# Optimization experiments

Hardware: AMD Instinct MI355X
Metric: run time of the kernel (lower is better)

## Reference

```python
import jax, jax.numpy as jnp
import numpy as np

NUM_USER = 100000
NUM_ENTITY = 1000000
NUM_RELATION = 60
DIM = 32
N_NEIGHBOR = 16
N_ITER = 2
BATCH = 8192


def setup_inputs() -> dict:
    key = jax.random.key(0)
    ks = jax.random.split(key, 9)
    users = jax.random.randint(ks[0], (BATCH,), 0, NUM_USER)
    items = jax.random.randint(ks[1], (BATCH,), 0, NUM_ENTITY)
    entity_emb = jax.random.normal(ks[2], (NUM_ENTITY, DIM), dtype=jnp.float32) * 0.1
    relation_emb = jax.random.normal(ks[3], (NUM_RELATION, DIM), dtype=jnp.float32) * 0.1
    adj_entity = jax.random.randint(ks[4], (NUM_ENTITY, N_NEIGHBOR), 0, NUM_ENTITY)
    adj_relation = jax.random.randint(ks[5], (NUM_ENTITY, N_NEIGHBOR), 0, NUM_RELATION)
    user_history = jax.random.randint(ks[6], (NUM_USER, N_NEIGHBOR), 0, NUM_ENTITY)
    W = jax.random.normal(ks[7], (DIM, DIM), dtype=jnp.float32) / np.sqrt(DIM)
    b = jnp.zeros((DIM,), dtype=jnp.float32)
    return {"users": users, "items": items, "entity_emb": entity_emb,
            "relation_emb": relation_emb, "adj_entity": adj_entity,
            "adj_relation": adj_relation, "user_history": user_history,
            "W": W, "b": b}


def reference(users, items, entity_emb, relation_emb, adj_entity, adj_relation, user_history, W, b):
    B = users.shape[0]
    d = entity_emb.shape[1]
    K = adj_entity.shape[1]

    # user embedding: mean-pool over gathered history item embeddings
    hist = user_history[users]                         # [B, K]
    user_emb = entity_emb[hist].mean(axis=1)           # [B, d]

    # multi-hop neighbor expansion (irregular gathers)
    entities = [items.reshape(B, 1)]
    relations = []
    for h in range(N_ITER):
        e = adj_entity[entities[h]].reshape(B, -1)     # [B, K^(h+1)]
        r = adj_relation[entities[h]].reshape(B, -1)
        entities.append(e)
        relations.append(r)

    ent_vecs = [entity_emb[e] for e in entities]       # hop h: [B, K^h, d]
    rel_vecs = [relation_emb[r] for r in relations]

    def aggregate(self_v, neigh_v, neigh_r, act):
        # self_v: [B, n, d]; neigh_v/neigh_r: [B, n, K, d]
        scores = jnp.einsum('bd,bnkd->bnk', user_emb, neigh_r)
        attn = jax.nn.softmax(scores, axis=-1)          # softmax over K neighbors
        agg = jnp.einsum('bnk,bnkd->bnd', attn, neigh_v)
        return act((self_v + agg) @ W + b)

    for it in range(N_ITER):
        act = jnp.tanh if it == N_ITER - 1 else jax.nn.sigmoid
        ent_vecs = [
            aggregate(ent_vecs[h],
                      ent_vecs[h + 1].reshape(B, -1, K, d),
                      rel_vecs[h].reshape(B, -1, K, d),
                      act)
            for h in range(N_ITER - it)
        ]

    item_emb = ent_vecs[0].reshape(B, d)
    scores = jnp.sum(user_emb * item_emb, axis=1)
    return jax.nn.sigmoid(scores)
```

## Files before the change

### kernel.cpp

```cpp
#include <hip/hip_runtime.h>
#include <hip/hip_bf16.h>


#define DIMV 32
#define KN   16
#define NREL 60
#define NT   256

__device__ __forceinline__ float sigmoidf_(float x) { return 1.0f / (1.0f + __expf(-x)); }

__global__ __launch_bounds__(NT) void mkgcn_fused(
    const int* __restrict__ users,
    const int* __restrict__ items,
    const float* __restrict__ E,
    const float* __restrict__ R,
    const int* __restrict__ adjE,
    const int* __restrict__ adjR,
    const int* __restrict__ uhist,
    const float* __restrict__ Wg,
    const float* __restrict__ bg,
    float* __restrict__ out)
{
    const int b = blockIdx.x;
    const int t = threadIdx.x;

    __shared__ float ue[DIMV];
    __shared__ float sdot[NREL];
    __shared__ int   e1[KN];
    __shared__ int   r1[KN];
    __shared__ int   e2off[256];
    __shared__ int   r2[256];
    __shared__ float v1[KN][DIMV];
    __shared__ float attn2[256];
    __shared__ float attn0[KN];
    __shared__ float x1[KN][DIMV];
    __shared__ float hv1[KN][DIMV];
    __shared__ float Wl[DIMV][DIMV];
    __shared__ float bl[DIMV];
    __shared__ float part[8][DIMV];
    __shared__ int   hrow[KN];
    __shared__ float v0[DIMV];
    __shared__ float x0[DIMV];
    __shared__ float h0[DIMV];

    const int user = users[b];
    const int item = items[b];

    if (t < KN) {
        hrow[t] = uhist[(long)user * KN + t];
    } else if (t < 2 * KN) {
        e1[t - KN] = adjE[(long)item * KN + (t - KN)];
    } else if (t < 3 * KN) {
        r1[t - 2 * KN] = adjR[(long)item * KN + (t - 2 * KN)];
    } else if (t >= 64 && t < 96) {
        v0[t - 64] = E[(long)item * DIMV + (t - 64)];
        bl[t - 64] = bg[t - 64];
    }
    {
        float* wflat = &Wl[0][0];
        #pragma unroll
        for (int i = t; i < DIMV * DIMV; i += NT) wflat[i] = Wg[i];
    }
    __syncthreads();

    {
        const int r = t >> 5, d = t & 31;
        part[r][d] = E[(long)hrow[r] * DIMV + d] + E[(long)hrow[r + 8] * DIMV + d];
    }
    {
        const int n = t >> 4, k = t & 15;
        const long base = (long)e1[n] * KN + k;
        e2off[t] = adjE[base] * DIMV;
        r2[t]    = adjR[base];
    }
    #pragma unroll
    for (int i = t; i < KN * DIMV; i += NT) {
        const int row = i >> 5, d = i & 31;
        v1[row][d] = E[(long)e1[row] * DIMV + d];
    }
    __syncthreads();

    if (t < DIMV) {
        float s = 0.f;
        #pragma unroll
        for (int r = 0; r < 8; r++) s += part[r][t];
        ue[t] = s * (1.0f / 16.0f);
    }
    __syncthreads();

    if (t < NREL) {
        const float* rr = R + t * DIMV;
        float s = 0.f;
        #pragma unroll
        for (int d = 0; d < DIMV; d++) s += ue[d] * rr[d];
        sdot[t] = s;
    }
    __syncthreads();

    {
        float s = sdot[r2[t]];
        float m = s;
        #pragma unroll
        for (int off = 1; off < 16; off <<= 1) m = fmaxf(m, __shfl_xor(m, off, 16));
        float e = __expf(s - m);
        float sum = e;
        #pragma unroll
        for (int off = 1; off < 16; off <<= 1) sum += __shfl_xor(sum, off, 16);
        attn2[t] = e / sum;
    }
    if (t < KN) {
        float s = sdot[r1[t]];
        float m = s;
        #pragma unroll
        for (int off = 1; off < 16; off <<= 1) m = fmaxf(m, __shfl_xor(m, off, 16));
        float e = __expf(s - m);
        float sum = e;
        #pragma unroll
        for (int off = 1; off < 16; off <<= 1) sum += __shfl_xor(sum, off, 16);
        attn0[t] = e / sum;
    }
    __syncthreads();

    #pragma unroll
    for (int p = 0; p < 2; p++) {
        const int n = (t >> 5) + 8 * p;
        const int d = t & 31;
        const int base = n * KN;
        float acc = 0.f;
        #pragma unroll
        for (int k = 0; k < KN; k++) {
            acc += attn2[base + k] * E[(long)e2off[base + k] + d];
        }
        x1[n][d] = v1[n][d] + acc;
    }
    __syncthreads();

    #pragma unroll
    for (int p = 0; p < 2; p++) {
        const int n = (t >> 5) + 8 * p;
        const int dp = t & 31;
        float acc = bl[dp];
        #pragma unroll
        for (int d = 0; d < DIMV; d++) acc += x1[n][d] * Wl[d][dp];
        hv1[n][dp] = sigmoidf_(acc);
    }
    __syncthreads();

    if (t < DIMV) {
        float a = 0.f;
        #pragma unroll
        for (int k = 0; k < KN; k++) a += attn0[k] * v1[k][t];
        x0[t] = v0[t] + a;
    }
    __syncthreads();

    if (t < DIMV) {
        float acc = bl[t];
        #pragma unroll
        for (int d = 0; d < DIMV; d++) acc += x0[d] * Wl[d][t];
        h0[t] = sigmoidf_(acc);
    }
    __syncthreads();

    if (t < DIMV) {
        float a = 0.f;
        #pragma unroll
        for (int k = 0; k < KN; k++) a += attn0[k] * hv1[k][t];
        x0[t] = h0[t] + a;
    }
    __syncthreads();

    if (t < DIMV) {
        float acc = bl[t];
        #pragma unroll
        for (int d = 0; d < DIMV; d++) acc += x0[d] * Wl[d][t];
        const float ie = tanhf(acc);
        float p = ue[t] * ie;
        #pragma unroll
        for (int off = 1; off < 32; off <<= 1) p += __shfl_xor(p, off, 32);
        if (t == 0) out[b] = sigmoidf_(p);
    }
}

extern "C" void kernel_launch(void* const* d_in, const int* in_sizes, int n_in,
                              void* d_out, int out_size, void* d_ws, size_t ws_size,
                              hipStream_t stream) {
    const int* users   = (const int*)d_in[0];
    const int* items   = (const int*)d_in[1];
    const float* E     = (const float*)d_in[2];
    const float* R     = (const float*)d_in[3];
    const int* adjE    = (const int*)d_in[4];
    const int* adjR    = (const int*)d_in[5];
    const int* uhist   = (const int*)d_in[6];
    const float* Wg    = (const float*)d_in[7];
    const float* bg    = (const float*)d_in[8];
    float* out         = (float*)d_out;

    const int B = in_sizes[0];
    mkgcn_fused<<<B, NT, 0, stream>>>(users, items, E, R, adjE, adjR, uhist, Wg, bg, out);
}
```

Measured before the change: 293.5 us.

## Vectorize gathers with float4/int4 and split hop-2 aggregation across thread pairs

Replaces scalar per-element gathers of embeddings, adjacency rows and W with float4/int4 loads spread over thread groups. The hop-2 weighted sum now has each thread load float4 slices for half of the 16 neighbors, then combines the pair with a shuffle. Also adds an occupancy hint to launch_bounds and aligns shared arrays. The intent is fewer memory instructions and wider gather transactions, at the cost of more register pressure and some idle lanes.

```diff
diff --git a/kernel.cpp b/kernel.cpp
--- a/kernel.cpp
+++ b/kernel.cpp
@@ -9,7 +9,7 @@
 
 __device__ __forceinline__ float sigmoidf_(float x) { return 1.0f / (1.0f + __expf(-x)); }
 
-__global__ __launch_bounds__(NT) void mkgcn_fused(
+__global__ __launch_bounds__(NT, 8) void mkgcn_fused(
     const int* __restrict__ users,
     const int* __restrict__ items,
     const float* __restrict__ E,
@@ -24,22 +24,22 @@
     const int b = blockIdx.x;
     const int t = threadIdx.x;
 
+    __shared__ __align__(16) float Wl[DIMV][DIMV];
+    __shared__ __align__(16) float v1s[KN][DIMV];
+    __shared__ __align__(16) float x1s[KN][DIMV];
+    __shared__ __align__(16) float hv1[KN][DIMV];
+    __shared__ __align__(16) float part[8][DIMV];
+    __shared__ int   e2[256];
+    __shared__ int   r2[256];
+    __shared__ float attn2[256];
     __shared__ float ue[DIMV];
     __shared__ float sdot[NREL];
+    __shared__ float attn0[KN];
     __shared__ int   e1[KN];
     __shared__ int   r1[KN];
-    __shared__ int   e2off[256];
-    __shared__ int   r2[256];
-    __shared__ float v1[KN][DIMV];
-    __shared__ float attn2[256];
-    __shared__ float attn0[KN];
-    __shared__ float x1[KN][DIMV];
-    __shared__ float hv1[KN][DIMV];
-    __shared__ float Wl[DIMV][DIMV];
+    __shared__ int   hrow[KN];
     __shared__ float bl[DIMV];
-    __shared__ float part[8][DIMV];
-    __shared__ int   hrow[KN];
-    __shared__ float v0[DIMV];
+    __shared__ float v0c[DIMV];
     __shared__ float x0[DIMV];
     __shared__ float h0[DIMV];
 
@@ -53,30 +53,37 @@
     } else if (t < 3 * KN) {
         r1[t - 2 * KN] = adjR[(long)item * KN + (t - 2 * KN)];
     } else if (t >= 64 && t < 96) {
-        v0[t - 64] = E[(long)item * DIMV + (t - 64)];
-        bl[t - 64] = bg[t - 64];
-    }
-    {
-        float* wflat = &Wl[0][0];
-        #pragma unroll
-        for (int i = t; i < DIMV * DIMV; i += NT) wflat[i] = Wg[i];
-    }
-    __syncthreads();
-
-    {
-        const int r = t >> 5, d = t & 31;
-        part[r][d] = E[(long)hrow[r] * DIMV + d] + E[(long)hrow[r + 8] * DIMV + d];
-    }
-    {
-        const int n = t >> 4, k = t & 15;
-        const long base = (long)e1[n] * KN + k;
-        e2off[t] = adjE[base] * DIMV;
-        r2[t]    = adjR[base];
-    }
-    #pragma unroll
-    for (int i = t; i < KN * DIMV; i += NT) {
-        const int row = i >> 5, d = i & 31;
-        v1[row][d] = E[(long)e1[row] * DIMV + d];
+        v0c[t - 64] = E[(long)item * DIMV + (t - 64)];
+        bl[t - 64]  = bg[t - 64];
+    }
+    ((float4*)Wl)[t] = ((const float4*)Wg)[t];
+    __syncthreads();
+
+    if (t < 64) {
+        const int r = t >> 3, v = t & 7;
+        const float4 a = ((const float4*)(E + (long)hrow[r] * DIMV))[v];
+        const float4 c = ((const float4*)(E + (long)hrow[r + 8] * DIMV))[v];
+        float4 s; s.x = a.x + c.x; s.y = a.y + c.y; s.z = a.z + c.z; s.w = a.w + c.w;
+        ((float4*)part)[t] = s;
+    } else if (t < 128) {
+        const int i = t - 64;
+        const int n = i >> 2, c = i & 3;
+        ((int4*)e2)[i] = ((const int4*)(adjE + (long)e1[n] * KN))[c];
+    } else if (t < 192) {
+        const int i = t - 128;
+        const int n = i >> 2, c = i & 3;
+        ((int4*)r2)[i] = ((const int4*)(adjR + (long)e1[n] * KN))[c];
+    } else {
+        const int i = t - 192;
+        {
+            const int n = i >> 3, v = i & 7;
+            ((float4*)v1s)[i] = ((const float4*)(E + (long)e1[n] * DIMV))[v];
+        }
+        {
+            const int s = i + 64;
+            const int n = s >> 3, v = s & 7;
+            ((float4*)v1s)[s] = ((const float4*)(E + (long)e1[n] * DIMV))[v];
+        }
     }
     __syncthreads();
 
@@ -121,17 +128,29 @@
     }
     __syncthreads();
 
-    #pragma unroll
-    for (int p = 0; p < 2; p++) {
-        const int n = (t >> 5) + 8 * p;
-        const int d = t & 31;
-        const int base = n * KN;
-        float acc = 0.f;
-        #pragma unroll
-        for (int k = 0; k < KN; k++) {
-            acc += attn2[base + k] * E[(long)e2off[base + k] + d];
-        }
-        x1[n][d] = v1[n][d] + acc;
+    {
+        const int n  = t >> 4;
+        const int v  = (t >> 1) & 7;
+        const int kh = t & 1;
+        const int base = n * KN + kh * 8;
+        float4 acc = make_float4(0.f, 0.f, 0.f, 0.f);
+        #pragma unroll
+        for (int k = 0; k < 8; k++) {
+            const int row = e2[base + k];
+            const float a = attn2[base + k];
+            const float4 f = ((const float4*)(E + (long)row * DIMV))[v];
+            acc.x += a * f.x; acc.y += a * f.y; acc.z += a * f.z; acc.w += a * f.w;
+        }
+        acc.x += __shfl_xor(acc.x, 1);
+        acc.y += __shfl_xor(acc.y, 1);
+        acc.z += __shfl_xor(acc.z, 1);
+        acc.w += __shfl_xor(acc.w, 1);
+        if (kh == 0) {
+            const float4 vv = ((float4*)v1s)[n * 8 + v];
+            float4 r; r.x = vv.x + acc.x; r.y = vv.y + acc.y;
+            r.z = vv.z + acc.z; r.w = vv.w + acc.w;
+            ((float4*)x1s)[n * 8 + v] = r;
+        }
     }
     __syncthreads();
 
@@ -141,7 +160,7 @@
         const int dp = t & 31;
         float acc = bl[dp];
         #pragma unroll
-        for (int d = 0; d < DIMV; d++) acc += x1[n][d] * Wl[d][dp];
+        for (int d = 0; d < DIMV; d++) acc += x1s[n][d] * Wl[d][dp];
         hv1[n][dp] = sigmoidf_(acc);
     }
     __syncthreads();
@@ -149,8 +168,8 @@
     if (t < DIMV) {
         float a = 0.f;
         #pragma unroll
-        for (int k = 0; k < KN; k++) a += attn0[k] * v1[k][t];
-        x0[t] = v0[t] + a;
+        for (int k = 0; k < KN; k++) a += attn0[k] * v1s[k][t];
+        x0[t] = v0c[t] + a;
     }
     __syncthreads();
 
```

After: 300.4 us. 1.02x slower.

## Process one batch element per wavefront with vectorized float4 gathers

Applied to the files above, without the earlier changes.

Restructures the kernel so each 64-lane wavefront handles one batch element, four per block, instead of one 256-thread block per element. Index broadcasts now use shuffles, and embedding rows are gathered with float4/int4 loads. Shared buffers such as x1 are reused for the relation indices and the hop-1 outputs, and W is loaded once per block. This cuts per-element thread count and memory transactions. The cost is less parallelism per element for the 256-neighbor gather, and block-wide syncthreads still couple the four elements.

```diff
diff --git a/kernel.cpp b/kernel.cpp
--- a/kernel.cpp
+++ b/kernel.cpp
@@ -1,15 +1,11 @@
 #include <hip/hip_runtime.h>
-#include <hip/hip_bf16.h>
-
-
-#define DIMV 32
-#define KN   16
-#define NREL 60
-#define NT   256
+
+
+#define NT 256
 
 __device__ __forceinline__ float sigmoidf_(float x) { return 1.0f / (1.0f + __expf(-x)); }
 
-__global__ __launch_bounds__(NT) void mkgcn_fused(
+__global__ __launch_bounds__(NT) void mkgcn_wpe(
     const int* __restrict__ users,
     const int* __restrict__ items,
     const float* __restrict__ E,
@@ -19,166 +15,197 @@
     const int* __restrict__ uhist,
     const float* __restrict__ Wg,
     const float* __restrict__ bg,
-    float* __restrict__ out)
+    float* __restrict__ out,
+    int B)
 {
-    const int b = blockIdx.x;
+    struct PE {
+        int   e2[256];
+        float attn[256];
+        float v1[16][32];
+        float x1[16][32];
+        float ue[32];
+        float sdot[64];
+        float attn0[16];
+        float v0[32];
+        float x0[32];
+        float h0[32];
+    };
+    __shared__ __align__(16) float Wl[32][32];
+    __shared__ float bl[32];
+    __shared__ __align__(16) PE pe[4];
+
     const int t = threadIdx.x;
-
-    __shared__ float ue[DIMV];
-    __shared__ float sdot[NREL];
-    __shared__ int   e1[KN];
-    __shared__ int   r1[KN];
-    __shared__ int   e2off[256];
-    __shared__ int   r2[256];
-    __shared__ float v1[KN][DIMV];
-    __shared__ float attn2[256];
-    __shared__ float attn0[KN];
-    __shared__ float x1[KN][DIMV];
-    __shared__ float hv1[KN][DIMV];
-    __shared__ float Wl[DIMV][DIMV];
-    __shared__ float bl[DIMV];
-    __shared__ float part[8][DIMV];
-    __shared__ int   hrow[KN];
-    __shared__ float v0[DIMV];
-    __shared__ float x0[DIMV];
-    __shared__ float h0[DIMV];
+    const int w = t >> 6;
+    const int L = t & 63;
+    int b = blockIdx.x * 4 + w;
+    if (b >= B) b = B - 1;
+    PE& P = pe[w];
 
     const int user = users[b];
     const int item = items[b];
 
-    if (t < KN) {
-        hrow[t] = uhist[(long)user * KN + t];
-    } else if (t < 2 * KN) {
-        e1[t - KN] = adjE[(long)item * KN + (t - KN)];
-    } else if (t < 3 * KN) {
-        r1[t - 2 * KN] = adjR[(long)item * KN + (t - 2 * KN)];
-    } else if (t >= 64 && t < 96) {
-        v0[t - 64] = E[(long)item * DIMV + (t - 64)];
-        bl[t - 64] = bg[t - 64];
-    }
-    {
-        float* wflat = &Wl[0][0];
-        #pragma unroll
-        for (int i = t; i < DIMV * DIMV; i += NT) wflat[i] = Wg[i];
-    }
-    __syncthreads();
-
-    {
-        const int r = t >> 5, d = t & 31;
-        part[r][d] = E[(long)hrow[r] * DIMV + d] + E[(long)hrow[r + 8] * DIMV + d];
-    }
-    {
-        const int n = t >> 4, k = t & 15;
-        const long base = (long)e1[n] * KN + k;
-        e2off[t] = adjE[base] * DIMV;
-        r2[t]    = adjR[base];
+    int hid = 0, e1v = 0, r1v = 0;
+    if (L < 16)       hid = uhist[(long)user * 16 + L];
+    else if (L < 32)  e1v = adjE[(long)item * 16 + (L - 16)];
+    else if (L < 48)  r1v = adjR[(long)item * 16 + (L - 32)];
+    else if (L < 56)  ((float4*)P.v0)[L - 48] = ((const float4*)(E + (long)item * 32))[L - 48];
+    ((float4*)Wl)[t] = ((const float4*)Wg)[t];
+    if (t < 32) bl[t] = bg[t];
+
+    const int v  = L & 7;
+    const int r8 = L >> 3;
+
+    {
+        const int h0i = __shfl(hid, r8);
+        const int h1i = __shfl(hid, r8 + 8);
+        const float4 a = ((const float4*)(E + (long)h0i * 32))[v];
+        const float4 c = ((const float4*)(E + (long)h1i * 32))[v];
+        float sx = a.x + c.x, sy = a.y + c.y, sz = a.z + c.z, sw = a.w + c.w;
+        #pragma unroll
+        for (int off = 8; off < 64; off <<= 1) {
+            sx += __shfl_xor(sx, off); sy += __shfl_xor(sy, off);
+            sz += __shfl_xor(sz, off); sw += __shfl_xor(sw, off);
+        }
+        if (L < 8) {
+            float4 u; u.x = sx * 0.0625f; u.y = sy * 0.0625f;
+            u.z = sz * 0.0625f; u.w = sw * 0.0625f;
+            ((float4*)P.ue)[L] = u;
+        }
+    }
+    {
+        const int n = L >> 2, c4 = L & 3;
+        const int e1n = __shfl(e1v, 16 + n);
+        const int4 ev = ((const int4*)(adjE + (long)e1n * 16))[c4];
+        const int4 rv = ((const int4*)(adjR + (long)e1n * 16))[c4];
+        int* x1i = (int*)P.x1;
+        P.e2[(c4 * 4 + 0) * 16 + n] = ev.x;  P.e2[(c4 * 4 + 1) * 16 + n] = ev.y;
+        P.e2[(c4 * 4 + 2) * 16 + n] = ev.z;  P.e2[(c4 * 4 + 3) * 16 + n] = ev.w;
+        x1i[(c4 * 4 + 0) * 16 + n] = rv.x;   x1i[(c4 * 4 + 1) * 16 + n] = rv.y;
+        x1i[(c4 * 4 + 2) * 16 + n] = rv.z;   x1i[(c4 * 4 + 3) * 16 + n] = rv.w;
     }
     #pragma unroll
-    for (int i = t; i < KN * DIMV; i += NT) {
-        const int row = i >> 5, d = i & 31;
-        v1[row][d] = E[(long)e1[row] * DIMV + d];
-    }
-    __syncthreads();
-
-    if (t < DIMV) {
+    for (int it = 0; it < 2; ++it) {
+        const int r = r8 + 8 * it;
+        const int e1r = __shfl(e1v, 16 + r);
+        ((float4*)P.v1)[r * 8 + v] = ((const float4*)(E + (long)e1r * 32))[v];
+    }
+    __syncthreads();
+
+    if (L < 60) {
+        const float4* rr = (const float4*)(R + L * 32);
+        const float4* uu = (const float4*)P.ue;
         float s = 0.f;
         #pragma unroll
-        for (int r = 0; r < 8; r++) s += part[r][t];
-        ue[t] = s * (1.0f / 16.0f);
-    }
-    __syncthreads();
-
-    if (t < NREL) {
-        const float* rr = R + t * DIMV;
-        float s = 0.f;
-        #pragma unroll
-        for (int d = 0; d < DIMV; d++) s += ue[d] * rr[d];
-        sdot[t] = s;
-    }
-    __syncthreads();
-
-    {
-        float s = sdot[r2[t]];
+        for (int j = 0; j < 8; ++j) {
+            const float4 a = rr[j], u = uu[j];
+            s += a.x * u.x + a.y * u.y + a.z * u.z + a.w * u.w;
+        }
+        P.sdot[L] = s;
+    }
+    __syncthreads();
+
+    {
+        const int* r2T = (const int*)P.x1;
+        #pragma unroll
+        for (int c = 0; c < 4; ++c) {
+            const int k = L & 15, n = c * 4 + (L >> 4);
+            const float s = P.sdot[r2T[k * 16 + n]];
+            float m = s;
+            #pragma unroll
+            for (int off = 1; off < 16; off <<= 1) m = fmaxf(m, __shfl_xor(m, off, 16));
+            const float e = __expf(s - m);
+            float sum = e;
+            #pragma unroll
+            for (int off = 1; off < 16; off <<= 1) sum += __shfl_xor(sum, off, 16);
+            P.attn[k * 16 + n] = e / sum;
+        }
+    }
+    const int r1L = __shfl(r1v, 32 + (L & 15));
+    if (L < 16) {
+        const float s = P.sdot[r1L];
         float m = s;
         #pragma unroll
         for (int off = 1; off < 16; off <<= 1) m = fmaxf(m, __shfl_xor(m, off, 16));
-        float e = __expf(s - m);
+        const float e = __expf(s - m);
         float sum = e;
         #pragma unroll
         for (int off = 1; off < 16; off <<= 1) sum += __shfl_xor(sum, off, 16);
-        attn2[t] = e / sum;
-    }
-    if (t < KN) {
-        float s = sdot[r1[t]];
-        float m = s;
-        #pragma unroll
-        for (int off = 1; off < 16; off <<= 1) m = fmaxf(m, __shfl_xor(m, off, 16));
-        float e = __expf(s - m);
-        float sum = e;
-        #pragma unroll
-        for (int off = 1; off < 16; off <<= 1) sum += __shfl_xor(sum, off, 16);
-        attn0[t] = e / sum;
-    }
-    __syncthreads();
-
-    #pragma unroll
-    for (int p = 0; p < 2; p++) {
-        const int n = (t >> 5) + 8 * p;
-        const int d = t & 31;
-        const int base = n * KN;
-        float acc = 0.f;
-        #pragma unroll
-        for (int k = 0; k < KN; k++) {
-            acc += attn2[base + k] * E[(long)e2off[base + k] + d];
-        }
-        x1[n][d] = v1[n][d] + acc;
-    }
-    __syncthreads();
-
-    #pragma unroll
-    for (int p = 0; p < 2; p++) {
-        const int n = (t >> 5) + 8 * p;
-        const int dp = t & 31;
-        float acc = bl[dp];
-        #pragma unroll
-        for (int d = 0; d < DIMV; d++) acc += x1[n][d] * Wl[d][dp];
-        hv1[n][dp] = sigmoidf_(acc);
-    }
-    __syncthreads();
-
-    if (t < DIMV) {
+        P.attn0[L] = e / sum;
+    }
+    __syncthreads();
+
+    {
+        const int n  = L >> 2;
+        const int s0 = (L & 3) * 2;
+        float ax0 = 0, ay0 = 0, az0 = 0, aw0 = 0;
+        float ax1 = 0, ay1 = 0, az1 = 0, aw1 = 0;
+        #pragma unroll 4
+        for (int k = 0; k < 16; ++k) {
+            const int   row = P.e2[k * 16 + n];
+            const float aw  = P.attn[k * 16 + n];
+            const float4* er = (const float4*)(E + (long)row * 32);
+            const float4 f0 = er[s0];
+            const float4 f1 = er[s0 + 1];
+            ax0 += aw * f0.x; ay0 += aw * f0.y; az0 += aw * f0.z; aw0 += aw * f0.w;
+            ax1 += aw * f1.x; ay1 += aw * f1.y; az1 += aw * f1.z; aw1 += aw * f1.w;
+        }
+        const float4 va = ((const float4*)P.v1)[n * 8 + s0];
+        const float4 vb = ((const float4*)P.v1)[n * 8 + s0 + 1];
+        float4 xa, xb;
+        xa.x = va.x + ax0; xa.y = va.y + ay0; xa.z = va.z + az0; xa.w = va.w + aw0;
+        xb.x = vb.x + ax1; xb.y = vb.y + ay1; xb.z = vb.z + az1; xb.w = vb.w + aw1;
+        ((float4*)P.x1)[n * 8 + s0]     = xa;
+        ((float4*)P.x1)[n * 8 + s0 + 1] = xb;
+    }
+    __syncthreads();
+
+    const int dp = L & 31, half = L >> 5;
+    {
+        float hv[8];
+        #pragma unroll
+        for (int p = 0; p < 8; ++p) {
+            const int n = p * 2 + half;
+            float acc = bl[dp];
+            #pragma unroll
+            for (int d = 0; d < 32; ++d) acc += P.x1[n][d] * Wl[d][dp];
+            hv[p] = sigmoidf_(acc);
+        }
+        #pragma unroll
+        for (int p = 0; p < 8; ++p) P.x1[p * 2 + half][dp] = hv[p];
+    }
+    if (L < 32) {
         float a = 0.f;
         #pragma unroll
-        for (int k = 0; k < KN; k++) a += attn0[k] * v1[k][t];
-        x0[t] = v0[t] + a;
-    }
-    __syncthreads();
-
-    if (t < DIMV) {
-        float acc = bl[t];
-        #pragma unroll
-        for (int d = 0; d < DIMV; d++) acc += x0[d] * Wl[d][t];
-        h0[t] = sigmoidf_(acc);
-    }
-    __syncthreads();
-
-    if (t < DIMV) {
+        for (int k = 0; k < 16; ++k) a += P.attn0[k] * P.v1[k][L];
+        P.x0[L] = P.v0[L] + a;
+    }
+    __syncthreads();
+
+    if (L < 32) {
+        float acc = bl[L];
+        #pragma unroll
+        for (int d = 0; d < 32; ++d) acc += P.x0[d] * Wl[d][L];
+        P.h0[L] = sigmoidf_(acc);
+    }
+    __syncthreads();
+
+    if (L < 32) {
         float a = 0.f;
         #pragma unroll
-        for (int k = 0; k < KN; k++) a += attn0[k] * hv1[k][t];
-        x0[t] = h0[t] + a;
-    }
-    __syncthreads();
-
-    if (t < DIMV) {
-        float acc = bl[t];
-        #pragma unroll
-        for (int d = 0; d < DIMV; d++) acc += x0[d] * Wl[d][t];
+        for (int k = 0; k < 16; ++k) a += P.attn0[k] * P.x1[k][L];
+        P.x0[L] = P.h0[L] + a;
+    }
+    __syncthreads();
+
+    if (L < 32) {
+        float acc = bl[L];
+        #pragma unroll
+        for (int d = 0; d < 32; ++d) acc += P.x0[d] * Wl[d][L];
         const float ie = tanhf(acc);
-        float p = ue[t] * ie;
-        #pragma unroll
-        for (int off = 1; off < 32; off <<= 1) p += __shfl_xor(p, off, 32);
-        if (t == 0) out[b] = sigmoidf_(p);
+        float pr = P.ue[L] * ie;
+        #pragma unroll
+        for (int off = 1; off < 32; off <<= 1) pr += __shfl_xor(pr, off, 32);
+        if (L == 0) out[b] = sigmoidf_(pr);
     }
 }
 
@@ -197,5 +224,6 @@
     float* out         = (float*)d_out;
 
     const int B = in_sizes[0];
-    mkgcn_fused<<<B, NT, 0, stream>>>(users, items, E, R, adjE, adjR, uhist, Wg, bg, out);
+    const int grid = (B + 3) / 4;
+    mkgcn_wpe<<<grid, NT, 0, stream>>>(users, items, E, R, adjE, adjR, uhist, Wg, bg, out, B);
 }
```

New measurement: 284.1 us. 3.2% less time.
